# Optimization experiments

Hardware: AMD Instinct MI355X
Metric: run time of the kernel (lower is better)

Reference implementation:

```python
import jax, jax.numpy as jnp
import numpy as np

N_PATCH, N_Z, K, BS = 16, 128, 10, 1024
D = N_PATCH * N_Z


def setup_inputs() -> dict:
    key = jax.random.key(0)
    k1, k2, k3, k4 = jax.random.split(key, 4)
    z = jax.random.normal(k1, (BS, D), dtype=jnp.float32)
    m = jax.random.normal(k2, (K, D), dtype=jnp.float32)
    L = jax.random.normal(k3, (K, D, D), dtype=jnp.float32)
    components = jax.random.randint(k4, (BS,), 0, K, dtype=jnp.int64)
    return {"z": z, "m": m, "L": L, "components": components}


def reference(z, m, L, components):
    # samps[k] = m[k] + z @ L[k].T   -> (K, BS, D)
    samps = jnp.einsum('bd,ked->kbe', z, L) + m[:, None, :]
    # one-hot mask-and-sum over components == gather selected expert per sample
    x = samps[components, jnp.arange(z.shape[0])]  # (BS, D)
    return x.reshape(-1, N_PATCH, N_Z)
```

## Files before the change

kernel.cpp:

```cpp
#include <hip/hip_runtime.h>
#include <hip/hip_bf16.h>


#define DDIM  2048
#define BSAMP 1024
#define KCOMP 10
#define MPAD  160
#define NT    32
#define BK    32
#define NITER (DDIM / BK)
#define TILEB (MPAD * BK * 2)
#define ABYTES TILEB
#define BBYTES (NT * BK * 4)
#define STAGE_BYTES (ABYTES + BBYTES)

typedef __attribute__((ext_vector_type(8))) short bf16x8;
typedef __attribute__((ext_vector_type(4))) float f32x4;

__device__ __forceinline__ void async16(void* lds, const void* g) {
    __builtin_amdgcn_global_load_lds(
        (const __attribute__((address_space(1))) void*)g,
        (__attribute__((address_space(3))) void*)lds, 16, 0, 0);
}

__device__ __forceinline__ short bfs(float x) {
    __hip_bfloat16 h = __float2bfloat16(x);
    return *reinterpret_cast<short*>(&h);
}

__global__ void build_map(const int* __restrict__ comp,
                          int* __restrict__ rowmap,
                          int* __restrict__ counts) {
    __shared__ int sc[KCOMP];
    const int t = threadIdx.x;
    if (t < KCOMP) sc[t] = 0;
    __syncthreads();
    const int c = comp[t];
    const int r = atomicAdd(&sc[c], 1);
    if (r < MPAD) rowmap[c * MPAD + r] = t;
    __syncthreads();
    if (t < KCOMP) counts[t] = sc[t];
}

__global__ void zgather(const float* __restrict__ z,
                        const int* __restrict__ rowmap,
                        short* __restrict__ zb) {
    const int k  = blockIdx.x;
    const int sp = blockIdx.y;
    const int t  = threadIdx.x;
    const int c  = t & 7;
    const int g  = c & 3;
    const int s0 = rowmap[k * MPAD + 2 * sp]     & (BSAMP - 1);
    const int s1 = rowmap[k * MPAD + 2 * sp + 1] & (BSAMP - 1);
    const int src = (c >> 2) ? s1 : s0;
    const int swz = (c ^ (sp & 7)) * 16;
    char* kbase = (char*)zb + (size_t)k * NITER * TILEB + sp * 128 + swz;
#pragma unroll
    for (int p = 0; p < 2; ++p) {
        const int it = p * 32 + (t >> 3);
        const float* zr = z + (size_t)src * DDIM + it * BK + g * 8;
        f32x4 x = *(const f32x4*)zr;
        f32x4 y = *(const f32x4*)(zr + 4);
        bf16x8 r;
#pragma unroll
        for (int i = 0; i < 4; ++i) { r[i] = bfs(x[i]); r[4 + i] = bfs(y[i]); }
        *(bf16x8*)(kbase + (size_t)it * TILEB) = r;
    }
}

__global__ __launch_bounds__(256, 4)
void gmm_gemm(const short* __restrict__ zb,
              const float* __restrict__ mvec,
              const float* __restrict__ Lmat,
              const int* __restrict__ rowmap,
              const int* __restrict__ counts,
              float* __restrict__ out) {
    __shared__ __attribute__((aligned(16))) char smem[2 * STAGE_BYTES];
    const int t    = threadIdx.x;
    const int lane = t & 63;
    const int w    = t >> 6;
    const int mh   = w >> 1;
    const int nh   = w & 1;
    const int k    = blockIdx.y;
    const int n0   = blockIdx.x * NT;
    const float* Lk = Lmat + (size_t)k * DDIM * DDIM;
    const char* zt  = (const char*)zb + (size_t)k * NITER * TILEB;
    const int cnt  = counts[k];

    int mtmax = (cnt - mh * 80 + 15) >> 4;
    mtmax = mtmax < 0 ? 0 : (mtmax > 5 ? 5 : mtmax);

    const int br = t >> 3,          bc = ((t & 7) ^ (br & 7)) * 4;
    const unsigned ub = (unsigned)(t & ~63) * 16;

    auto stage = [&](int buf, int it) {
        char* lb = smem + buf * STAGE_BYTES;
        const char* at = zt + (size_t)it * TILEB;
        async16(lb + ub,        at + t * 16);
        async16(lb + 4096 + ub, at + 4096 + t * 16);
        if (t < 128)
            async16(lb + 8192 + ub, at + 8192 + t * 16);
        async16(lb + ABYTES + ub,
                Lk + (size_t)(n0 + br) * DDIM + it * BK + bc);
    };

    f32x4 acc[5];
#pragma unroll
    for (int mt = 0; mt < 5; ++mt) acc[mt] = (f32x4){0.f, 0.f, 0.f, 0.f};

    stage(0, 0);
    __syncthreads();

    const int fr = lane & 15;
    const int g  = lane >> 4;
    const int rb = nh * 16 + fr;
    const int h0 = ((2 * g)     ^ (rb & 7)) * 4;
    const int h1 = ((2 * g + 1) ^ (rb & 7)) * 4;
    const int frh = fr >> 1;
    const int fra = (fr & 1) * 4 + g;
    const int abase = (mh * 40 + frh) * 128 + ((fra ^ frh) * 16);

    for (int it = 0; it < NITER; ++it) {
        if (it + 1 < NITER) stage((it + 1) & 1, it + 1);
        const char* lb = smem + (it & 1) * STAGE_BYTES;
        const float* B = (const float*)(lb + ABYTES);

        f32x4 x = *(const f32x4*)(B + rb * 32 + h0);
        f32x4 y = *(const f32x4*)(B + rb * 32 + h1);
        bf16x8 bb;
#pragma unroll
        for (int i = 0; i < 4; ++i) { bb[i] = bfs(x[i]); bb[4 + i] = bfs(y[i]); }

#pragma unroll
        for (int mt = 0; mt < 5; ++mt) {
            if (mt < mtmax) {
                bf16x8 a = *(const bf16x8*)(lb + abase + mt * 1024);
                acc[mt] = __builtin_amdgcn_mfma_f32_16x16x32_bf16(a, bb, acc[mt], 0, 0, 0);
            }
        }
        __syncthreads();
    }

    const int rquad = g * 4;
    const int e  = n0 + nh * 16 + fr;
    const float mu = mvec[k * DDIM + e];
#pragma unroll
    for (int mt = 0; mt < 5; ++mt) {
        if (mt < mtmax) {
            const int sb = mh * 80 + mt * 16 + rquad;
#pragma unroll
            for (int r = 0; r < 4; ++r) {
                const int slot = sb + r;
                if (slot < cnt) {
                    const int b = rowmap[k * MPAD + slot];
                    out[(size_t)b * DDIM + e] = acc[mt][r] + mu;
                }
            }
        }
    }
}

extern "C" void kernel_launch(void* const* d_in, const int* in_sizes, int n_in,
                              void* d_out, int out_size, void* d_ws, size_t ws_size,
                              hipStream_t stream) {
    const float* z    = (const float*)d_in[0];
    const float* mvec = (const float*)d_in[1];
    const float* Lmat = (const float*)d_in[2];
    const int* comp   = (const int*)d_in[3];
    float* out        = (float*)d_out;

    int* rowmap = (int*)d_ws;
    int* counts = rowmap + KCOMP * MPAD;
    short* zb   = (short*)((char*)d_ws + 8192);

    build_map<<<1, BSAMP, 0, stream>>>(comp, rowmap, counts);
    zgather<<<dim3(KCOMP, MPAD / 2), 256, 0, stream>>>(z, rowmap, zb);
    gmm_gemm<<<dim3(DDIM / NT, KCOMP), 256, 0, stream>>>(zb, mvec, Lmat,
                                                         rowmap, counts, out);
}
```

Baseline: 269.5 us.

## Preload 16-row L stripe as bf16 in LDS, stream A from global

Each workgroup now owns a 16-row stripe of L for one component. At the start it loads the whole stripe (16x2048) into LDS, converting to bf16 with a swizzled layout. The gathered z tiles are then streamed straight from global/L2 into registers with double buffering, and the per-iteration syncthreads are gone. Workgroups are also remapped across XCDs, and 4 waves split the 10 M-tiles. The cost is a 64KB LDS footprint, which lowers occupancy to 2, plus a serial preload phase before any MFMA work starts.

Measured after the change: 330.5 us. 22.7% more time.

```diff
diff --git a/kernel.cpp b/kernel.cpp
--- a/kernel.cpp
+++ b/kernel.cpp
@@ -6,22 +6,16 @@
 #define BSAMP 1024
 #define KCOMP 10
 #define MPAD  160
-#define NT    32
 #define BK    32
 #define NITER (DDIM / BK)
-#define TILEB (MPAD * BK * 2)
-#define ABYTES TILEB
-#define BBYTES (NT * BK * 4)
-#define STAGE_BYTES (ABYTES + BBYTES)
+#define TILEB 10240
+#define STRIPES 128
+#define NWG   (KCOMP * STRIPES)
+#define NXCD  8
 
 typedef __attribute__((ext_vector_type(8))) short bf16x8;
+typedef __attribute__((ext_vector_type(4))) short s16x4;
 typedef __attribute__((ext_vector_type(4))) float f32x4;
-
-__device__ __forceinline__ void async16(void* lds, const void* g) {
-    __builtin_amdgcn_global_load_lds(
-        (const __attribute__((address_space(1))) void*)g,
-        (__attribute__((address_space(3))) void*)lds, 16, 0, 0);
-}
 
 __device__ __forceinline__ short bfs(float x) {
     __hip_bfloat16 h = __float2bfloat16(x);
@@ -68,92 +62,94 @@
     }
 }
 
-__global__ __launch_bounds__(256, 4)
+__global__ __launch_bounds__(256, 2)
 void gmm_gemm(const short* __restrict__ zb,
               const float* __restrict__ mvec,
               const float* __restrict__ Lmat,
               const int* __restrict__ rowmap,
               const int* __restrict__ counts,
               float* __restrict__ out) {
-    __shared__ __attribute__((aligned(16))) char smem[2 * STAGE_BYTES];
+    __shared__ __attribute__((aligned(16))) short Bs[16 * 2048];
+    char* Bb = (char*)Bs;
     const int t    = threadIdx.x;
     const int lane = t & 63;
     const int w    = t >> 6;
-    const int mh   = w >> 1;
-    const int nh   = w & 1;
-    const int k    = blockIdx.y;
-    const int n0   = blockIdx.x * NT;
-    const float* Lk = Lmat + (size_t)k * DDIM * DDIM;
+    const int lin  = blockIdx.x;
+    const int newlin = (lin & (NXCD - 1)) * (NWG / NXCD) + (lin >> 3);
+    const int k      = newlin >> 7;
+    const int stripe = newlin & (STRIPES - 1);
+    const int r0     = stripe * 16;
     const char* zt  = (const char*)zb + (size_t)k * NITER * TILEB;
     const int cnt  = counts[k];
 
-    int mtmax = (cnt - mh * 80 + 15) >> 4;
-    mtmax = mtmax < 0 ? 0 : (mtmax > 5 ? 5 : mtmax);
+    const f32x4* Ls = (const f32x4*)(Lmat + (size_t)k * DDIM * DDIM +
+                                     (size_t)r0 * DDIM);
+#pragma unroll
+    for (int j = 0; j < 32; ++j) {
+        const int idx = j * 256 + t;
+        f32x4 v = Ls[idx];
+        const int r  = idx >> 9;
+        const int cc = idx & 511;
+        s16x4 h = (s16x4){bfs(v[0]), bfs(v[1]), bfs(v[2]), bfs(v[3])};
+        *(s16x4*)(Bb + r * 4096 + ((cc ^ ((r & 7) << 1)) << 3)) = h;
+    }
+    __syncthreads();
 
-    const int br = t >> 3,          bc = ((t & 7) ^ (br & 7)) * 4;
-    const unsigned ub = (unsigned)(t & ~63) * 16;
+    const int fr  = lane & 15;
+    const int g   = lane >> 4;
+    const int fr2 = (fr & 7) << 1;
+    const int frh = fr >> 1;
+    const int fra = (fr & 1) * 4 + g;
+    const int abase = frh * 128 + ((fra ^ frh) * 16);
 
-    auto stage = [&](int buf, int it) {
-        char* lb = smem + buf * STAGE_BYTES;
-        const char* at = zt + (size_t)it * TILEB;
-        async16(lb + ub,        at + t * 16);
-        async16(lb + 4096 + ub, at + 4096 + t * 16);
-        if (t < 128)
-            async16(lb + 8192 + ub, at + 8192 + t * 16);
-        async16(lb + ABYTES + ub,
-                Lk + (size_t)(n0 + br) * DDIM + it * BK + bc);
+    bool act[3];
+    const char* ap[3];
+#pragma unroll
+    for (int i = 0; i < 3; ++i) {
+        const int mt = w + 4 * i;
+        act[i] = (mt < 10) && (mt * 16 < cnt);
+        ap[i]  = zt + mt * 1024 + abase;
+    }
+
+    f32x4 acc[3];
+#pragma unroll
+    for (int i = 0; i < 3; ++i) acc[i] = (f32x4){0.f, 0.f, 0.f, 0.f};
+
+    bf16x8 aE[3], aO[3];
+    auto loadA = [&](bf16x8 (&a)[3], int it) {
+#pragma unroll
+        for (int i = 0; i < 3; ++i)
+            if (act[i]) a[i] = *(const bf16x8*)(ap[i] + (size_t)it * TILEB);
+    };
+    auto step = [&](int it, bf16x8 (&a)[3]) {
+        bf16x8 b = *(const bf16x8*)(Bb + fr * 4096 +
+                                    (((it * 8 + 2 * g) ^ fr2) << 3));
+#pragma unroll
+        for (int i = 0; i < 3; ++i)
+            if (act[i])
+                acc[i] = __builtin_amdgcn_mfma_f32_16x16x32_bf16(a[i], b, acc[i], 0, 0, 0);
     };
 
-    f32x4 acc[5];
-#pragma unroll
-    for (int mt = 0; mt < 5; ++mt) acc[mt] = (f32x4){0.f, 0.f, 0.f, 0.f};
-
-    stage(0, 0);
-    __syncthreads();
-
-    const int fr = lane & 15;
-    const int g  = lane >> 4;
-    const int rb = nh * 16 + fr;
-    const int h0 = ((2 * g)     ^ (rb & 7)) * 4;
-    const int h1 = ((2 * g + 1) ^ (rb & 7)) * 4;
-    const int frh = fr >> 1;
-    const int fra = (fr & 1) * 4 + g;
-    const int abase = (mh * 40 + frh) * 128 + ((fra ^ frh) * 16);
-
-    for (int it = 0; it < NITER; ++it) {
-        if (it + 1 < NITER) stage((it + 1) & 1, it + 1);
-        const char* lb = smem + (it & 1) * STAGE_BYTES;
-        const float* B = (const float*)(lb + ABYTES);
-
-        f32x4 x = *(const f32x4*)(B + rb * 32 + h0);
-        f32x4 y = *(const f32x4*)(B + rb * 32 + h1);
-        bf16x8 bb;
-#pragma unroll
-        for (int i = 0; i < 4; ++i) { bb[i] = bfs(x[i]); bb[4 + i] = bfs(y[i]); }
-
-#pragma unroll
-        for (int mt = 0; mt < 5; ++mt) {
-            if (mt < mtmax) {
-                bf16x8 a = *(const bf16x8*)(lb + abase + mt * 1024);
-                acc[mt] = __builtin_amdgcn_mfma_f32_16x16x32_bf16(a, bb, acc[mt], 0, 0, 0);
-            }
-        }
-        __syncthreads();
+    loadA(aE, 0);
+    for (int it = 0; it < NITER; it += 2) {
+        loadA(aO, it + 1);
+        step(it, aE);
+        if (it + 2 < NITER) loadA(aE, it + 2);
+        step(it + 1, aO);
     }
 
-    const int rquad = g * 4;
-    const int e  = n0 + nh * 16 + fr;
+    const int e  = r0 + fr;
     const float mu = mvec[k * DDIM + e];
 #pragma unroll
-    for (int mt = 0; mt < 5; ++mt) {
-        if (mt < mtmax) {
-            const int sb = mh * 80 + mt * 16 + rquad;
+    for (int i = 0; i < 3; ++i) {
+        if (act[i]) {
+            const int sb = (w + 4 * i) * 16 + g * 4;
 #pragma unroll
             for (int r = 0; r < 4; ++r) {
                 const int slot = sb + r;
                 if (slot < cnt) {
                     const int b = rowmap[k * MPAD + slot];
-                    out[(size_t)b * DDIM + e] = acc[mt][r] + mu;
+                    out[(size_t)b * DDIM + e] = acc[i][r] + mu;
                 }
             }
         }
@@ -175,6 +171,5 @@
 
     build_map<<<1, BSAMP, 0, stream>>>(comp, rowmap, counts);
     zgather<<<dim3(KCOMP, MPAD / 2), 256, 0, stream>>>(z, rowmap, zb);
-    gmm_gemm<<<dim3(DDIM / NT, KCOMP), 256, 0, stream>>>(zb, mvec, Lmat,
-                                                         rowmap, counts, out);
+    gmm_gemm<<<NWG, 256, 0, stream>>>(zb, mvec, Lmat, rowmap, counts, out);
 }
```

## Widen N tile to 128 and split the reduction dimension four ways with atomic accumulation

Applied to the files above, without the earlier changes.

The GEMM tile grows from 32 to 128 output columns per workgroup, so each A-fragment load from LDS now feeds four MFMAs. The D reduction is split across 4 workgroups, with partial sums combined through atomicAdd into the output, which zgather now zero-fills. The grid becomes 640 workgroups of 16 iterations each instead of 640 of 64. The cost is atomic traffic on the output, a larger LDS footprint, higher register use (launch bounds lowered to 2), and a result that depends on floating-point summation order.

After: 317.6 us. +17.8%, slower.

```diff
diff --git a/kernel.cpp b/kernel.cpp
--- a/kernel.cpp
+++ b/kernel.cpp
@@ -6,13 +6,15 @@
 #define BSAMP 1024
 #define KCOMP 10
 #define MPAD  160
-#define NT    32
+#define NT    128
 #define BK    32
-#define NITER (DDIM / BK)
-#define TILEB (MPAD * BK * 2)
-#define ABYTES TILEB
-#define BBYTES (NT * BK * 4)
-#define STAGE_BYTES (ABYTES + BBYTES)
+#define SPLITS 4
+#define NS    16
+#define TILEB 10240
+#define ALDS  12288
+#define BLDS  16384
+#define STAGE_BYTES (ALDS + BLDS)
+#define NWG   (KCOMP * 16 * SPLITS)
 
 typedef __attribute__((ext_vector_type(8))) short bf16x8;
 typedef __attribute__((ext_vector_type(4))) float f32x4;
@@ -44,17 +46,26 @@
 
 __global__ void zgather(const float* __restrict__ z,
                         const int* __restrict__ rowmap,
-                        short* __restrict__ zb) {
+                        short* __restrict__ zb,
+                        float* __restrict__ out) {
     const int k  = blockIdx.x;
     const int sp = blockIdx.y;
     const int t  = threadIdx.x;
+    const int zid = k * (MPAD / 2) + sp;
+    if (zid < 512) {
+        float* o = out + (size_t)zid * 4096;
+        const f32x4 zero = (f32x4){0.f, 0.f, 0.f, 0.f};
+#pragma unroll
+        for (int j = 0; j < 4; ++j)
+            *(f32x4*)(o + (j * 256 + t) * 4) = zero;
+    }
     const int c  = t & 7;
     const int g  = c & 3;
     const int s0 = rowmap[k * MPAD + 2 * sp]     & (BSAMP - 1);
     const int s1 = rowmap[k * MPAD + 2 * sp + 1] & (BSAMP - 1);
     const int src = (c >> 2) ? s1 : s0;
     const int swz = (c ^ (sp & 7)) * 16;
-    char* kbase = (char*)zb + (size_t)k * NITER * TILEB + sp * 128 + swz;
+    char* kbase = (char*)zb + (size_t)k * 64 * TILEB + sp * 128 + swz;
 #pragma unroll
     for (int p = 0; p < 2; ++p) {
         const int it = p * 32 + (t >> 3);
@@ -68,7 +79,7 @@
     }
 }
 
-__global__ __launch_bounds__(256, 4)
+__global__ __launch_bounds__(256, 2)
 void gmm_gemm(const short* __restrict__ zb,
               const float* __restrict__ mvec,
               const float* __restrict__ Lmat,
@@ -81,79 +92,105 @@
     const int w    = t >> 6;
     const int mh   = w >> 1;
     const int nh   = w & 1;
-    const int k    = blockIdx.y;
-    const int n0   = blockIdx.x * NT;
+    const int bid  = blockIdx.x;
+    const int s    = bid & 3;
+    const int n0   = ((bid >> 2) & 15) * NT;
+    const int k    = bid >> 6;
+    const int ts   = s * NS;
+    const int d0b  = s * 512;
     const float* Lk = Lmat + (size_t)k * DDIM * DDIM;
-    const char* zt  = (const char*)zb + (size_t)k * NITER * TILEB;
+    const char* zt  = (const char*)zb + (size_t)k * 64 * TILEB;
     const int cnt  = counts[k];
 
     int mtmax = (cnt - mh * 80 + 15) >> 4;
     mtmax = mtmax < 0 ? 0 : (mtmax > 5 ? 5 : mtmax);
 
-    const int br = t >> 3,          bc = ((t & 7) ^ (br & 7)) * 4;
+    const int ac2 = (512 + t < 640) ? (512 + t) : 639;
+    int brr[4], bcc[4];
+#pragma unroll
+    for (int j = 0; j < 4; ++j) {
+        const int c = j * 256 + t;
+        brr[j] = c >> 3;
+        bcc[j] = (((c & 7) ^ (brr[j] & 7)) * 4);
+    }
     const unsigned ub = (unsigned)(t & ~63) * 16;
 
     auto stage = [&](int buf, int it) {
         char* lb = smem + buf * STAGE_BYTES;
-        const char* at = zt + (size_t)it * TILEB;
+        const char* at = zt + (size_t)(ts + it) * TILEB;
         async16(lb + ub,        at + t * 16);
         async16(lb + 4096 + ub, at + 4096 + t * 16);
-        if (t < 128)
-            async16(lb + 8192 + ub, at + 8192 + t * 16);
-        async16(lb + ABYTES + ub,
-                Lk + (size_t)(n0 + br) * DDIM + it * BK + bc);
+        async16(lb + 8192 + ub, at + ac2 * 16);
+        const int d0 = d0b + it * BK;
+#pragma unroll
+        for (int j = 0; j < 4; ++j)
+            async16(lb + ALDS + j * 4096 + ub,
+                    Lk + (size_t)(n0 + brr[j]) * DDIM + d0 + bcc[j]);
     };
 
-    f32x4 acc[5];
-#pragma unroll
-    for (int mt = 0; mt < 5; ++mt) acc[mt] = (f32x4){0.f, 0.f, 0.f, 0.f};
+    f32x4 acc[5][4];
+#pragma unroll
+    for (int mt = 0; mt < 5; ++mt)
+#pragma unroll
+        for (int q = 0; q < 4; ++q) acc[mt][q] = (f32x4){0.f, 0.f, 0.f, 0.f};
 
     stage(0, 0);
     __syncthreads();
 
     const int fr = lane & 15;
     const int g  = lane >> 4;
-    const int rb = nh * 16 + fr;
-    const int h0 = ((2 * g)     ^ (rb & 7)) * 4;
-    const int h1 = ((2 * g + 1) ^ (rb & 7)) * 4;
+    const int h0 = ((2 * g)     ^ (fr & 7)) * 4;
+    const int h1 = ((2 * g + 1) ^ (fr & 7)) * 4;
     const int frh = fr >> 1;
     const int fra = (fr & 1) * 4 + g;
     const int abase = (mh * 40 + frh) * 128 + ((fra ^ frh) * 16);
 
-    for (int it = 0; it < NITER; ++it) {
-        if (it + 1 < NITER) stage((it + 1) & 1, it + 1);
+    for (int it = 0; it < NS; ++it) {
+        if (it + 1 < NS) stage((it + 1) & 1, it + 1);
         const char* lb = smem + (it & 1) * STAGE_BYTES;
-        const float* B = (const float*)(lb + ABYTES);
-
-        f32x4 x = *(const f32x4*)(B + rb * 32 + h0);
-        f32x4 y = *(const f32x4*)(B + rb * 32 + h1);
-        bf16x8 bb;
-#pragma unroll
-        for (int i = 0; i < 4; ++i) { bb[i] = bfs(x[i]); bb[4 + i] = bfs(y[i]); }
-
+        const float* B = (const float*)(lb + ALDS);
+
+        bf16x8 bb[4];
+#pragma unroll
+        for (int q = 0; q < 4; ++q) {
+            const int rb = nh * 64 + q * 16 + fr;
+            f32x4 x = *(const f32x4*)(B + rb * 32 + h0);
+            f32x4 y = *(const f32x4*)(B + rb * 32 + h1);
+#pragma unroll
+            for (int i = 0; i < 4; ++i) {
+                bb[q][i]     = bfs(x[i]);
+                bb[q][4 + i] = bfs(y[i]);
+            }
+        }
 #pragma unroll
         for (int mt = 0; mt < 5; ++mt) {
             if (mt < mtmax) {
                 bf16x8 a = *(const bf16x8*)(lb + abase + mt * 1024);
-                acc[mt] = __builtin_amdgcn_mfma_f32_16x16x32_bf16(a, bb, acc[mt], 0, 0, 0);
+#pragma unroll
+                for (int q = 0; q < 4; ++q)
+                    acc[mt][q] = __builtin_amdgcn_mfma_f32_16x16x32_bf16(a, bb[q], acc[mt][q], 0, 0, 0);
             }
         }
         __syncthreads();
     }
 
     const int rquad = g * 4;
-    const int e  = n0 + nh * 16 + fr;
-    const float mu = mvec[k * DDIM + e];
-#pragma unroll
-    for (int mt = 0; mt < 5; ++mt) {
-        if (mt < mtmax) {
-            const int sb = mh * 80 + mt * 16 + rquad;
-#pragma unroll
-            for (int r = 0; r < 4; ++r) {
-                const int slot = sb + r;
-                if (slot < cnt) {
-                    const int b = rowmap[k * MPAD + slot];
-                    out[(size_t)b * DDIM + e] = acc[mt][r] + mu;
+#pragma unroll
+    for (int q = 0; q < 4; ++q) {
+        const int e = n0 + nh * 64 + q * 16 + fr;
+        const float mu = (s == 0) ? mvec[k * DDIM + e] : 0.f;
+#pragma unroll
+        for (int mt = 0; mt < 5; ++mt) {
+            if (mt < mtmax) {
+                const int sb = mh * 80 + mt * 16 + rquad;
+#pragma unroll
+                for (int r = 0; r < 4; ++r) {
+                    const int slot = sb + r;
+                    if (slot < cnt) {
+                        const int b = rowmap[k * MPAD + slot];
+                        atomicAdd(&out[(size_t)b * DDIM + e],
+                                  acc[mt][q][r] + mu);
+                    }
                 }
             }
         }
@@ -174,7 +211,6 @@
     short* zb   = (short*)((char*)d_ws + 8192);
 
     build_map<<<1, BSAMP, 0, stream>>>(comp, rowmap, counts);
-    zgather<<<dim3(KCOMP, MPAD / 2), 256, 0, stream>>>(z, rowmap, zb);
-    gmm_gemm<<<dim3(DDIM / NT, KCOMP), 256, 0, stream>>>(zb, mvec, Lmat,
-                                                         rowmap, counts, out);
-}
+    zgather<<<dim3(KCOMP, MPAD / 2), 256, 0, stream>>>(z, rowmap, zb, out);
+    gmm_gemm<<<NWG, 256, 0, stream>>>(zb, mvec, Lmat, rowmap, counts, out);
+}
```
